# Kernel optimization log

Hardware: AMD Instinct MI355X
Metric: run time of the kernel (lower is better)

Reference implementation:

```python
import jax, jax.numpy as jnp
import numpy as np

N_NODES = 50000
N_EDGES = 800000
FEAT_DIM = 1024
EMBED_DIM = 128


def setup_inputs() -> dict:
    key = jax.random.key(0)
    k_x, k_w, k_r, k_c, k_v = jax.random.split(key, 5)
    x = jax.random.normal(k_x, (N_NODES, FEAT_DIM), dtype=jnp.float32)
    # xavier-uniform equivalent for weight [embed_dim, feat_dim]
    limit = float(np.sqrt(6.0 / (EMBED_DIM + FEAT_DIM)))
    weight = jax.random.uniform(k_w, (EMBED_DIM, FEAT_DIM), dtype=jnp.float32,
                                minval=-limit, maxval=limit)
    # sparse adjacency in COO form (row = destination, col = source)
    adj_row = jax.random.randint(k_r, (N_EDGES,), 0, N_NODES, dtype=jnp.int32)
    adj_col = jax.random.randint(k_c, (N_EDGES,), 0, N_NODES, dtype=jnp.int32)
    adj_vals = jax.random.uniform(k_v, (N_EDGES,), dtype=jnp.float32)
    return {"x": x, "weight": weight, "adj_row": adj_row,
            "adj_col": adj_col, "adj_vals": adj_vals}


def reference(x, weight, adj_row, adj_col, adj_vals):
    # Fused GeMM-SpMM: out = A @ (x @ W^T)
    h = jnp.einsum('nf,ef->ne', x, weight)          # [N, embed_dim] dense GEMM
    msgs = adj_vals[:, None] * h[adj_col]           # gather source rows, scale by edge weight
    out = jax.ops.segment_sum(msgs, adj_row, num_segments=N_NODES)  # scatter-add to dest rows
    return out
```

## Files before the change

### kernel.cpp

```cpp
#include <hip/hip_runtime.h>
#include <hip/hip_bf16.h>

#define FEAT 1024
#define EMBED 128
#define CAP 64
#define OVF_CAP 4096

typedef __attribute__((ext_vector_type(8))) short short8;
typedef __attribute__((ext_vector_type(4))) float floatx4;

__device__ inline ushort f2bf(float f) {
    __hip_bfloat16 h = __float2bfloat16(f);
    return *reinterpret_cast<ushort*>(&h);
}
__device__ inline float bfbits_lo(uint u) {
    uint v = u << 16; return *reinterpret_cast<float*>(&v);
}
__device__ inline float bfbits_hi(uint u) {
    uint v = u & 0xffff0000u; return *reinterpret_cast<float*>(&v);
}

__global__ void swizzle_weight_kernel(const float* __restrict__ w,
                                      ushort* __restrict__ wbs) {
    int gid = blockIdx.x * blockDim.x + threadIdx.x;
    int l = gid & 63;
    int t = (gid >> 6) & 7;
    int s = gid >> 9;
    int row = t * 16 + (l & 15);
    int col = s * 32 + (l >> 4) * 8;
    const float* src = w + (size_t)row * FEAT + col;
    float4 v0 = *(const float4*)(src);
    float4 v1 = *(const float4*)(src + 4);
    short8 o;
    o[0] = f2bf(v0.x); o[1] = f2bf(v0.y); o[2] = f2bf(v0.z); o[3] = f2bf(v0.w);
    o[4] = f2bf(v1.x); o[5] = f2bf(v1.y); o[6] = f2bf(v1.z); o[7] = f2bf(v1.w);
    *(short8*)(wbs + (size_t)gid * 8) = o;
}

__launch_bounds__(256, 4)
__global__ void gemm_xwT_kernel(const float* __restrict__ x,
                                const ushort* __restrict__ wbs,
                                ushort* __restrict__ hb, int n_nodes) {
    const int lane = threadIdx.x & 63;
    const int wave = threadIdx.x >> 6;
    const int q    = lane >> 4;
    const int m    = lane & 15;
    const int base = blockIdx.x * 64 + wave * 16;

    int row = base + m;
    int row_ld = row < n_nodes ? row : (n_nodes - 1);
    const float*  xp = x + (size_t)row_ld * FEAT + q * 8;
    const ushort* bp = wbs + lane * 8;

    floatx4 acc[8];
#pragma unroll
    for (int t = 0; t < 8; ++t) acc[t] = (floatx4)(0.0f);

    float4 a0 = *(const float4*)(xp);
    float4 a1 = *(const float4*)(xp + 4);

    for (int s = 0; s < 32; ++s) {
        float4 na0, na1;
        if (s < 31) {
            na0 = *(const float4*)(xp + (s + 1) * 32);
            na1 = *(const float4*)(xp + (s + 1) * 32 + 4);
        }
        const ushort* bs = bp + s * 4096;
        short8 bf[8];
#pragma unroll
        for (int t = 0; t < 8; ++t) bf[t] = *(const short8*)(bs + t * 512);

        short8 af;
        af[0] = f2bf(a0.x); af[1] = f2bf(a0.y);
        af[2] = f2bf(a0.z); af[3] = f2bf(a0.w);
        af[4] = f2bf(a1.x); af[5] = f2bf(a1.y);
        af[6] = f2bf(a1.z); af[7] = f2bf(a1.w);

#pragma unroll
        for (int t = 0; t < 8; ++t)
            acc[t] = __builtin_amdgcn_mfma_f32_16x16x32_bf16(af, bf[t], acc[t], 0, 0, 0);
        a0 = na0; a1 = na1;
    }

#pragma unroll
    for (int t = 0; t < 8; ++t) {
#pragma unroll
        for (int r = 0; r < 4; ++r) {
            int rr = base + q * 4 + r;
            if (rr < n_nodes)
                hb[(size_t)rr * EMBED + t * 16 + m] = f2bf(acc[t][r]);
        }
    }
}

__global__ void bucket_fill_kernel(const int* __restrict__ adj_row,
                                   const int* __restrict__ adj_col,
                                   const float* __restrict__ adj_vals,
                                   int* __restrict__ cnt,
                                   int2* __restrict__ bucket,
                                   int* __restrict__ ovf_cnt,
                                   int* __restrict__ ovf_list,
                                   int n_edges) {
    int e = blockIdx.x * blockDim.x + threadIdx.x;
    if (e >= n_edges) return;
    int r = adj_row[e];
    int slot = atomicAdd(&cnt[r], 1);
    if (slot < CAP) {
        bucket[(size_t)r * CAP + slot] = make_int2(adj_col[e], __float_as_int(adj_vals[e]));
    } else {
        int oi = atomicAdd(ovf_cnt, 1);
        if (oi < OVF_CAP) ovf_list[oi] = e;
    }
}

__launch_bounds__(256)
__global__ void gather_kernel(const int* __restrict__ cnt,
                              const int2* __restrict__ bucket,
                              const ushort* __restrict__ hb,
                              float* __restrict__ out, int n_nodes) {
    int node = blockIdx.x * 4 + (threadIdx.x >> 6);
    if (node >= n_nodes) return;
    int lane = threadIdx.x & 63;
    int c = cnt[node];
    if (c > CAP) c = CAP;
    const int2* bp = bucket + (size_t)node * CAP;

    float accx = 0.0f, accy = 0.0f;
    int j = 0;
    for (; j + 4 <= c; j += 4) {
        int4 e01 = *(const int4*)(bp + j);
        int4 e23 = *(const int4*)(bp + j + 2);
        uint u0 = *(const uint*)(hb + (size_t)e01.x * EMBED + lane * 2);
        uint u1 = *(const uint*)(hb + (size_t)e01.z * EMBED + lane * 2);
        uint u2 = *(const uint*)(hb + (size_t)e23.x * EMBED + lane * 2);
        uint u3 = *(const uint*)(hb + (size_t)e23.z * EMBED + lane * 2);
        float w0 = __int_as_float(e01.y), w1 = __int_as_float(e01.w);
        float w2 = __int_as_float(e23.y), w3 = __int_as_float(e23.w);
        accx = fmaf(w0, bfbits_lo(u0), accx);  accy = fmaf(w0, bfbits_hi(u0), accy);
        accx = fmaf(w1, bfbits_lo(u1), accx);  accy = fmaf(w1, bfbits_hi(u1), accy);
        accx = fmaf(w2, bfbits_lo(u2), accx);  accy = fmaf(w2, bfbits_hi(u2), accy);
        accx = fmaf(w3, bfbits_lo(u3), accx);  accy = fmaf(w3, bfbits_hi(u3), accy);
    }
    for (; j < c; ++j) {
        int2 ev = bp[j];
        uint u = *(const uint*)(hb + (size_t)ev.x * EMBED + lane * 2);
        float w = __int_as_float(ev.y);
        accx = fmaf(w, bfbits_lo(u), accx);
        accy = fmaf(w, bfbits_hi(u), accy);
    }
    *(float2*)(out + (size_t)node * EMBED + lane * 2) = make_float2(accx, accy);
}

__global__ void overflow_fixup_kernel(const int* __restrict__ ovf_cnt,
                                      const int* __restrict__ ovf_list,
                                      const int* __restrict__ adj_row,
                                      const int* __restrict__ adj_col,
                                      const float* __restrict__ adj_vals,
                                      const ushort* __restrict__ hb,
                                      float* __restrict__ out) {
    int n = *ovf_cnt;
    if (n > OVF_CAP) n = OVF_CAP;
    int f = threadIdx.x;
    for (int i = blockIdx.x; i < n; i += gridDim.x) {
        int e = ovf_list[i];
        uint us = hb[(size_t)adj_col[e] * EMBED + f];
        uint v = us << 16;
        atomicAdd(&out[(size_t)adj_row[e] * EMBED + f],
                  adj_vals[e] * *reinterpret_cast<float*>(&v));
    }
}

extern "C" void kernel_launch(void* const* d_in, const int* in_sizes, int n_in,
                              void* d_out, int out_size, void* d_ws, size_t ws_size,
                              hipStream_t stream) {
    const float* x        = (const float*)d_in[0];
    const float* w        = (const float*)d_in[1];
    const int*   adj_row  = (const int*)d_in[2];
    const int*   adj_col  = (const int*)d_in[3];
    const float* adj_vals = (const float*)d_in[4];

    const int n_nodes = in_sizes[0] / FEAT;
    const int n_edges = in_sizes[2];
    float* out = (float*)d_out;

    char* ws = (char*)d_ws;
    ushort* wbs = (ushort*)ws;
    size_t off = 262144;
    ushort* hb = (ushort*)(ws + off);
    off += (size_t)n_nodes * EMBED * sizeof(ushort);
    char* meta = ws + off;
    int* cnt      = (int*)meta;
    int* ovf_cnt  = (int*)(meta + (size_t)n_nodes * 4);
    int* ovf_list = ovf_cnt + 1;
    size_t meta_bytes = ((size_t)n_nodes * 4 + 4 + OVF_CAP * 4 + 15) & ~(size_t)15;
    int2* bucket = (int2*)(meta + meta_bytes);

    hipMemsetAsync(meta, 0, meta_bytes, stream);

    swizzle_weight_kernel<<<64, 256, 0, stream>>>(w, wbs);

    gemm_xwT_kernel<<<(n_nodes + 63) / 64, 256, 0, stream>>>(x, wbs, hb, n_nodes);

    bucket_fill_kernel<<<(n_edges + 255) / 256, 256, 0, stream>>>(
        adj_row, adj_col, adj_vals, cnt, bucket, ovf_cnt, ovf_list, n_edges);

    gather_kernel<<<(n_nodes + 3) / 4, 256, 0, stream>>>(cnt, bucket, hb, out, n_nodes);

    overflow_fixup_kernel<<<64, 128, 0, stream>>>(
        ovf_cnt, ovf_list, adj_row, adj_col, adj_vals, hb, out);
}
```

Measured before the change: 424.6 us.

## Compute two row fragments per wave in GEMM and unroll gather by eight

Each GEMM wave now computes 32 rows (two 16-row MFMA fragments) and reuses each loaded weight fragment for both, halving weight reloads per output row. The block shrinks to 128 threads with launch bounds (128,3). In the gather kernel, the node index is made wave-uniform with readfirstlane and the edge loop is unrolled to 8 loads in flight to improve memory-level parallelism. The GEMM change doubles accumulator registers, which may reduce occupancy.

```diff
diff --git a/kernel.cpp b/kernel.cpp
--- a/kernel.cpp
+++ b/kernel.cpp
@@ -37,7 +37,7 @@
     *(short8*)(wbs + (size_t)gid * 8) = o;
 }
 
-__launch_bounds__(256, 4)
+__launch_bounds__(128, 3)
 __global__ void gemm_xwT_kernel(const float* __restrict__ x,
                                 const ushort* __restrict__ wbs,
                                 ushort* __restrict__ hb, int n_nodes) {
@@ -45,50 +45,68 @@
     const int wave = threadIdx.x >> 6;
     const int q    = lane >> 4;
     const int m    = lane & 15;
-    const int base = blockIdx.x * 64 + wave * 16;
-
-    int row = base + m;
-    int row_ld = row < n_nodes ? row : (n_nodes - 1);
-    const float*  xp = x + (size_t)row_ld * FEAT + q * 8;
-    const ushort* bp = wbs + lane * 8;
-
-    floatx4 acc[8];
-#pragma unroll
-    for (int t = 0; t < 8; ++t) acc[t] = (floatx4)(0.0f);
-
-    float4 a0 = *(const float4*)(xp);
-    float4 a1 = *(const float4*)(xp + 4);
+    const int base = blockIdx.x * 64 + wave * 32;
+
+    int row0 = base + m;
+    int row1 = base + 16 + m;
+    int r0l = row0 < n_nodes ? row0 : (n_nodes - 1);
+    int r1l = row1 < n_nodes ? row1 : (n_nodes - 1);
+    const float*  xp0 = x + (size_t)r0l * FEAT + q * 8;
+    const float*  xp1 = x + (size_t)r1l * FEAT + q * 8;
+    const ushort* bp  = wbs + lane * 8;
+
+    floatx4 acc[2][8];
+#pragma unroll
+    for (int rf = 0; rf < 2; ++rf)
+#pragma unroll
+        for (int t = 0; t < 8; ++t) acc[rf][t] = (floatx4)(0.0f);
+
+    float4 a00 = *(const float4*)(xp0);
+    float4 a01 = *(const float4*)(xp0 + 4);
+    float4 a10 = *(const float4*)(xp1);
+    float4 a11 = *(const float4*)(xp1 + 4);
 
     for (int s = 0; s < 32; ++s) {
-        float4 na0, na1;
+        float4 n00, n01, n10, n11;
         if (s < 31) {
-            na0 = *(const float4*)(xp + (s + 1) * 32);
-            na1 = *(const float4*)(xp + (s + 1) * 32 + 4);
+            n00 = *(const float4*)(xp0 + (s + 1) * 32);
+            n01 = *(const float4*)(xp0 + (s + 1) * 32 + 4);
+            n10 = *(const float4*)(xp1 + (s + 1) * 32);
+            n11 = *(const float4*)(xp1 + (s + 1) * 32 + 4);
         }
         const ushort* bs = bp + s * 4096;
         short8 bf[8];
 #pragma unroll
         for (int t = 0; t < 8; ++t) bf[t] = *(const short8*)(bs + t * 512);
 
-        short8 af;
-        af[0] = f2bf(a0.x); af[1] = f2bf(a0.y);
-        af[2] = f2bf(a0.z); af[3] = f2bf(a0.w);
-        af[4] = f2bf(a1.x); af[5] = f2bf(a1.y);
-        af[6] = f2bf(a1.z); af[7] = f2bf(a1.w);
-
-#pragma unroll
-        for (int t = 0; t < 8; ++t)
-            acc[t] = __builtin_amdgcn_mfma_f32_16x16x32_bf16(af, bf[t], acc[t], 0, 0, 0);
-        a0 = na0; a1 = na1;
-    }
-
-#pragma unroll
-    for (int t = 0; t < 8; ++t) {
-#pragma unroll
-        for (int r = 0; r < 4; ++r) {
-            int rr = base + q * 4 + r;
-            if (rr < n_nodes)
-                hb[(size_t)rr * EMBED + t * 16 + m] = f2bf(acc[t][r]);
+        short8 af0, af1;
+        af0[0] = f2bf(a00.x); af0[1] = f2bf(a00.y);
+        af0[2] = f2bf(a00.z); af0[3] = f2bf(a00.w);
+        af0[4] = f2bf(a01.x); af0[5] = f2bf(a01.y);
+        af0[6] = f2bf(a01.z); af0[7] = f2bf(a01.w);
+        af1[0] = f2bf(a10.x); af1[1] = f2bf(a10.y);
+        af1[2] = f2bf(a10.z); af1[3] = f2bf(a10.w);
+        af1[4] = f2bf(a11.x); af1[5] = f2bf(a11.y);
+        af1[6] = f2bf(a11.z); af1[7] = f2bf(a11.w);
+
+#pragma unroll
+        for (int t = 0; t < 8; ++t) {
+            acc[0][t] = __builtin_amdgcn_mfma_f32_16x16x32_bf16(af0, bf[t], acc[0][t], 0, 0, 0);
+            acc[1][t] = __builtin_amdgcn_mfma_f32_16x16x32_bf16(af1, bf[t], acc[1][t], 0, 0, 0);
+        }
+        a00 = n00; a01 = n01; a10 = n10; a11 = n11;
+    }
+
+#pragma unroll
+    for (int rf = 0; rf < 2; ++rf) {
+#pragma unroll
+        for (int t = 0; t < 8; ++t) {
+#pragma unroll
+            for (int r = 0; r < 4; ++r) {
+                int rr = base + rf * 16 + q * 4 + r;
+                if (rr < n_nodes)
+                    hb[(size_t)rr * EMBED + t * 16 + m] = f2bf(acc[rf][t][r]);
+            }
         }
     }
 }
@@ -118,32 +136,53 @@
                               const int2* __restrict__ bucket,
                               const ushort* __restrict__ hb,
                               float* __restrict__ out, int n_nodes) {
-    int node = blockIdx.x * 4 + (threadIdx.x >> 6);
+    int node = __builtin_amdgcn_readfirstlane(blockIdx.x * 4 + (threadIdx.x >> 6));
     if (node >= n_nodes) return;
     int lane = threadIdx.x & 63;
     int c = cnt[node];
     if (c > CAP) c = CAP;
     const int2* bp = bucket + (size_t)node * CAP;
+    const ushort* hl = hb + lane * 2;
 
     float accx = 0.0f, accy = 0.0f;
     int j = 0;
-    for (; j + 4 <= c; j += 4) {
+    for (; j + 8 <= c; j += 8) {
         int4 e01 = *(const int4*)(bp + j);
         int4 e23 = *(const int4*)(bp + j + 2);
-        uint u0 = *(const uint*)(hb + (size_t)e01.x * EMBED + lane * 2);
-        uint u1 = *(const uint*)(hb + (size_t)e01.z * EMBED + lane * 2);
-        uint u2 = *(const uint*)(hb + (size_t)e23.x * EMBED + lane * 2);
-        uint u3 = *(const uint*)(hb + (size_t)e23.z * EMBED + lane * 2);
+        int4 e45 = *(const int4*)(bp + j + 4);
+        int4 e67 = *(const int4*)(bp + j + 6);
+        uint u0 = *(const uint*)(hl + (size_t)e01.x * EMBED);
+        uint u1 = *(const uint*)(hl + (size_t)e01.z * EMBED);
+        uint u2 = *(const uint*)(hl + (size_t)e23.x * EMBED);
+        uint u3 = *(const uint*)(hl + (size_t)e23.z * EMBED);
+        uint u4 = *(const uint*)(hl + (size_t)e45.x * EMBED);
+        uint u5 = *(const uint*)(hl + (size_t)e45.z * EMBED);
+        uint u6 = *(const uint*)(hl + (size_t)e67.x * EMBED);
+        uint u7 = *(const uint*)(hl + (size_t)e67.z * EMBED);
         float w0 = __int_as_float(e01.y), w1 = __int_as_float(e01.w);
         float w2 = __int_as_float(e23.y), w3 = __int_as_float(e23.w);
+        float w4 = __int_as_float(e45.y), w5 = __int_as_float(e45.w);
+        float w6 = __int_as_float(e67.y), w7 = __int_as_float(e67.w);
         accx = fmaf(w0, bfbits_lo(u0), accx);  accy = fmaf(w0, bfbits_hi(u0), accy);
         accx = fmaf(w1, bfbits_lo(u1), accx);  accy = fmaf(w1, bfbits_hi(u1), accy);
         accx = fmaf(w2, bfbits_lo(u2), accx);  accy = fmaf(w2, bfbits_hi(u2), accy);
         accx = fmaf(w3, bfbits_lo(u3), accx);  accy = fmaf(w3, bfbits_hi(u3), accy);
-    }
-    for (; j < c; ++j) {
+        accx = fmaf(w4, bfbits_lo(u4), accx);  accy = fmaf(w4, bfbits_hi(u4), accy);
+        accx = fmaf(w5, bfbits_lo(u5), accx);  accy = fmaf(w5, bfbits_hi(u5), accy);
+        accx = fmaf(w6, bfbits_lo(u6), accx);  accy = fmaf(w6, bfbits_hi(u6), accy);
+        accx = fmaf(w7, bfbits_lo(u7), accx);  accy = fmaf(w7, bfbits_hi(u7), accy);
+    }
+    for (; j + 2 <= c; j += 2) {
+        int4 e01 = *(const int4*)(bp + j);
+        uint u0 = *(const uint*)(hl + (size_t)e01.x * EMBED);
+        uint u1 = *(const uint*)(hl + (size_t)e01.z * EMBED);
+        float w0 = __int_as_float(e01.y), w1 = __int_as_float(e01.w);
+        accx = fmaf(w0, bfbits_lo(u0), accx);  accy = fmaf(w0, bfbits_hi(u0), accy);
+        accx = fmaf(w1, bfbits_lo(u1), accx);  accy = fmaf(w1, bfbits_hi(u1), accy);
+    }
+    if (j < c) {
         int2 ev = bp[j];
-        uint u = *(const uint*)(hb + (size_t)ev.x * EMBED + lane * 2);
+        uint u = *(const uint*)(hl + (size_t)ev.x * EMBED);
         float w = __int_as_float(ev.y);
         accx = fmaf(w, bfbits_lo(u), accx);
         accy = fmaf(w, bfbits_hi(u), accy);
@@ -199,7 +238,7 @@
 
     swizzle_weight_kernel<<<64, 256, 0, stream>>>(w, wbs);
 
-    gemm_xwT_kernel<<<(n_nodes + 63) / 64, 256, 0, stream>>>(x, wbs, hb, n_nodes);
+    gemm_xwT_kernel<<<(n_nodes + 63) / 64, 128, 0, stream>>>(x, wbs, hb, n_nodes);
 
     bucket_fill_kernel<<<(n_edges + 255) / 256, 256, 0, stream>>>(
         adj_row, adj_col, adj_vals, cnt, bucket, ovf_cnt, ovf_list, n_edges);
```

Result: faster. 408.5 us (-3.8%).
